# Kernel optimization log

Hardware: AMD Instinct MI355X
Metric: run time of the kernel (lower is better)

## Reference

```python
import jax, jax.numpy as jnp
import numpy as np

ALPHA = 0.2  # LeakyReLU negative slope


def setup_inputs() -> dict:
    key = jax.random.key(0)
    ks = jax.random.split(key, 7)
    N, D, O, R = 50000, 128, 128, 64
    E1, E2 = 800000, 200000
    return {
        "input": jax.random.normal(ks[0], (N, D), jnp.float32),
        "edge": jax.random.randint(ks[1], (2, E1), 0, N),
        "edge_embed": jax.random.normal(ks[2], (E1, R), jnp.float32),
        "edge_list_nhop": jax.random.randint(ks[3], (2, E2), 0, N),
        "edge_embed_nhop": jax.random.normal(ks[4], (E2, R), jnp.float32),
        "a": jax.random.normal(ks[5], (O, 2 * D + R), jnp.float32) * 0.05,
        "a_2": jax.random.normal(ks[6], (1, O), jnp.float32) * 0.05,
    }


def _gat_forward(x, edge, e_embed, a, a_2):
    N, D = x.shape
    src, dst = edge[0], edge[1]
    # a @ [x_src; x_dst; e_embed]^T computed blockwise (avoids [E, 2D+R] concat)
    a_src, a_dst, a_rel = a[:, :D], a[:, D:2 * D], a[:, 2 * D:]
    edge_m = x[src] @ a_src.T + x[dst] @ a_dst.T + e_embed @ a_rel.T  # [E, O] == edge_m^T
    score = edge_m @ a_2[0]                                            # [E]
    powers = -jnp.where(score > 0, score, ALPHA * score)               # -LeakyReLU
    edge_e = jnp.exp(powers)                                           # [E]
    e_rowsum = jax.ops.segment_sum(edge_e, src, num_segments=N)[:, None]  # [N, 1]
    e_rowsum = jnp.where(e_rowsum == 0.0, 1e-12, e_rowsum)
    edge_w = edge_e[:, None] * edge_m                                  # [E, O]
    h_prime = jax.ops.segment_sum(edge_w, src, num_segments=N)         # [N, O]
    h_prime = h_prime / e_rowsum
    return jax.nn.elu(h_prime)  # concat=True path


def reference(input, edge, edge_embed, edge_list_nhop, edge_embed_nhop, a, a_2):
    edge_all = jnp.concatenate([edge, edge_list_nhop], axis=1)        # [2, E1+E2]
    embed_all = jnp.concatenate([edge_embed, edge_embed_nhop], axis=0)  # [E1+E2, R]
    return _gat_forward(input, edge_all, embed_all, a, a_2)
```

## Files before the change

kernel.cpp:

```cpp
#include <hip/hip_runtime.h>
#include <hip/hip_bf16.h>

#define LRELU_ALPHA 0.2f

typedef __bf16 bf16x8 __attribute__((ext_vector_type(8)));
typedef float f32x4 __attribute__((ext_vector_type(4)));

__device__ __forceinline__ float waveReduceSum(float v) {
#pragma unroll
    for (int off = 32; off > 0; off >>= 1)
        v += __shfl_xor(v, off, 64);
    return v;
}

__global__ void k_prep(const float* __restrict__ a, const float* __restrict__ a2,
                       float* __restrict__ vall, __hip_bfloat16* __restrict__ ABf) {
    int idx = blockIdx.x * 256 + threadIdx.x;
    if (idx < 128 * 320) ABf[idx] = __float2bfloat16(a[idx]);
    if (idx < 320) {
        float s = 0.f;
#pragma unroll 8
        for (int o = 0; o < 128; ++o) s += a[o * 320 + idx] * a2[o];
        vall[idx] = s;
    }
}

__global__ void k_node_scores(const float* __restrict__ x, const float* __restrict__ vall,
                              float* __restrict__ s_src, float* __restrict__ s_dst,
                              __hip_bfloat16* __restrict__ XBf, int N) {
    int wid = (int)((blockIdx.x * (size_t)blockDim.x + threadIdx.x) >> 6);
    int lane = threadIdx.x & 63;
    if (wid >= N) return;
    const float* xp = x + (size_t)wid * 128;
    float x0 = xp[lane], x1 = xp[lane + 64];
    XBf[(size_t)wid * 128 + lane]      = __float2bfloat16(x0);
    XBf[(size_t)wid * 128 + 64 + lane] = __float2bfloat16(x1);
    float ps = x0 * vall[lane] + x1 * vall[lane + 64];
    float pd = x0 * vall[128 + lane] + x1 * vall[192 + lane];
    ps = waveReduceSum(ps);
    pd = waveReduceSum(pd);
    if (lane == 0) { s_src[wid] = ps; s_dst[wid] = pd; }
}

__global__ void k_count(const int* __restrict__ e1, int E1, const int* __restrict__ e2, int E2,
                        int* __restrict__ cnt) {
    int e = blockIdx.x * blockDim.x + threadIdx.x;
    if (e >= E1 + E2) return;
    int src = (e < E1) ? e1[e] : e2[e - E1];
    atomicAdd(&cnt[src], 1);
}

__global__ void k_scan1(const int* __restrict__ cnt, int* __restrict__ bsum, int N) {
    __shared__ int red[256];
    int t = threadIdx.x;
    int idx = blockIdx.x * 256 + t;
    red[t] = (idx < N) ? cnt[idx] : 0;
    __syncthreads();
    for (int off = 128; off > 0; off >>= 1) {
        if (t < off) red[t] += red[t + off];
        __syncthreads();
    }
    if (t == 0) bsum[blockIdx.x] = red[0];
}

__global__ void k_scan2(int* __restrict__ bsum, int nb) {
    __shared__ int tmp[256];
    int t = threadIdx.x;
    int v = (t < nb) ? bsum[t] : 0;
    tmp[t] = v;
    __syncthreads();
    for (int off = 1; off < 256; off <<= 1) {
        int add = (t >= off) ? tmp[t - off] : 0;
        __syncthreads();
        tmp[t] += add;
        __syncthreads();
    }
    if (t < nb) bsum[t] = tmp[t] - v;
}

__global__ void k_scan3(const int* __restrict__ cnt, const int* __restrict__ bsum,
                        int* __restrict__ start, int* __restrict__ cursor, int N, int E) {
    __shared__ int tmp[256];
    int t = threadIdx.x;
    int idx = blockIdx.x * 256 + t;
    int v = (idx < N) ? cnt[idx] : 0;
    tmp[t] = v;
    __syncthreads();
    for (int off = 1; off < 256; off <<= 1) {
        int add = (t >= off) ? tmp[t - off] : 0;
        __syncthreads();
        tmp[t] += add;
        __syncthreads();
    }
    if (idx < N) {
        int excl = tmp[t] - v + bsum[blockIdx.x];
        start[idx] = excl;
        cursor[idx] = excl;
    }
    if (blockIdx.x == 0 && t == 0) start[N] = E;
}

__global__ void k_scatter(const int* __restrict__ e1, int E1, const int* __restrict__ e2, int E2,
                          int* __restrict__ cursor, int2* __restrict__ se) {
    int e = blockIdx.x * blockDim.x + threadIdx.x;
    if (e >= E1 + E2) return;
    int src, dst;
    if (e < E1) { src = e1[e]; dst = e1[E1 + e]; }
    else { int t = e - E1; src = e2[t]; dst = e2[E2 + t]; }
    int p = atomicAdd(&cursor[src], 1);
    se[p] = make_int2(dst, e);
}

__global__ void k_gather(const __hip_bfloat16* __restrict__ XBf,
                         const float* __restrict__ emb1, const float* __restrict__ emb2, int E1,
                         const int* __restrict__ start, const int2* __restrict__ se,
                         const float* __restrict__ vall,
                         const float* __restrict__ s_src, const float* __restrict__ s_dst,
                         __hip_bfloat16* __restrict__ G, float* __restrict__ sxf, int N) {
    int n = (int)((blockIdx.x * (size_t)blockDim.x + threadIdx.x) >> 6);
    int lane = threadIdx.x & 63;
    if (n >= N) return;
    n = __builtin_amdgcn_readfirstlane(n);
    int b = start[n], en = start[n + 1];
    float r2l = vall[256 + lane];
    float ssrc = s_src[n];
    float ux = 0.f, uy = 0.f, w0 = 0.f, rs = 0.f;
    int p = b;
    for (; p + 1 < en; p += 2) {
        int2 d0 = se[p], d1 = se[p + 1];
        const float* ep0 = (d0.y < E1) ? emb1 + (size_t)d0.y * 64 : emb2 + (size_t)(d0.y - E1) * 64;
        const float* ep1 = (d1.y < E1) ? emb1 + (size_t)d1.y * 64 : emb2 + (size_t)(d1.y - E1) * 64;
        float em0 = ep0[lane], em1 = ep1[lane];
        __hip_bfloat162 xv0 = *reinterpret_cast<const __hip_bfloat162*>(XBf + (size_t)d0.x * 128 + 2 * lane);
        __hip_bfloat162 xv1 = *reinterpret_cast<const __hip_bfloat162*>(XBf + (size_t)d1.x * 128 + 2 * lane);
        float sd0 = s_dst[d0.x], sd1 = s_dst[d1.x];
        float t0 = em0 * r2l, t1 = em1 * r2l;
#pragma unroll
        for (int off = 32; off > 0; off >>= 1) {
            t0 += __shfl_xor(t0, off, 64);
            t1 += __shfl_xor(t1, off, 64);
        }
        float sc0 = ssrc + sd0 + t0;
        float sc1 = ssrc + sd1 + t1;
        float pz0 = sc0 > 0.f ? sc0 : LRELU_ALPHA * sc0;
        float pz1 = sc1 > 0.f ? sc1 : LRELU_ALPHA * sc1;
        float e0 = __expf(-pz0), e1v = __expf(-pz1);
        ux += e0 * __bfloat162float(xv0.x); uy += e0 * __bfloat162float(xv0.y);
        w0 += e0 * em0; rs += e0;
        ux += e1v * __bfloat162float(xv1.x); uy += e1v * __bfloat162float(xv1.y);
        w0 += e1v * em1; rs += e1v;
    }
    if (p < en) {
        int2 d0 = se[p];
        const float* ep0 = (d0.y < E1) ? emb1 + (size_t)d0.y * 64 : emb2 + (size_t)(d0.y - E1) * 64;
        float em0 = ep0[lane];
        __hip_bfloat162 xv0 = *reinterpret_cast<const __hip_bfloat162*>(XBf + (size_t)d0.x * 128 + 2 * lane);
        float sd0 = s_dst[d0.x];
        float t0 = waveReduceSum(em0 * r2l);
        float sc0 = ssrc + sd0 + t0;
        float pz0 = sc0 > 0.f ? sc0 : LRELU_ALPHA * sc0;
        float e0 = __expf(-pz0);
        ux += e0 * __bfloat162float(xv0.x); uy += e0 * __bfloat162float(xv0.y);
        w0 += e0 * em0; rs += e0;
    }
    float inv = (rs == 0.f) ? 0.f : 1.f / rs;
    __hip_bfloat16* gp = G + (size_t)n * 192;
    __hip_bfloat162 uv;
    uv.x = __float2bfloat16(ux * inv);
    uv.y = __float2bfloat16(uy * inv);
    *reinterpret_cast<__hip_bfloat162*>(gp + 2 * lane) = uv;
    gp[128 + lane] = __float2bfloat16(w0 * inv);
    if (lane == 0) sxf[n] = (rs == 0.f) ? 0.f : 1.f;
}

__global__ __launch_bounds__(256) void k_mfma(
    const __hip_bfloat16* __restrict__ XBf, const __hip_bfloat16* __restrict__ G,
    const __hip_bfloat16* __restrict__ ABf, const float* __restrict__ sxf,
    float* __restrict__ out, int N) {
    int lane = threadIdx.x & 63;
    int wave = threadIdx.x >> 6;
    int m0 = blockIdx.x * 64 + wave * 16;
    int q = lane >> 4, m = lane & 15;
    int rowm = m0 + m; if (rowm >= N) rowm = N - 1;
    const __hip_bfloat16* xr = XBf + (size_t)rowm * 128 + q * 8;
    const __hip_bfloat16* gr = G + (size_t)rowm * 192 + q * 8;
    const __hip_bfloat16* br = ABf + (size_t)m * 320 + q * 8;
    f32x4 acc[8];
#pragma unroll
    for (int c = 0; c < 8; ++c) acc[c] = f32x4{0.f, 0.f, 0.f, 0.f};

#pragma unroll
    for (int s = 0; s < 4; ++s) {
        bf16x8 af = *reinterpret_cast<const bf16x8*>(xr + s * 32);
#pragma unroll
        for (int c = 0; c < 8; ++c) {
            bf16x8 bf = *reinterpret_cast<const bf16x8*>(br + (size_t)c * 16 * 320 + s * 32);
            acc[c] = __builtin_amdgcn_mfma_f32_16x16x32_bf16(af, bf, acc[c], 0, 0, 0);
        }
    }
#pragma unroll
    for (int s = 0; s < 6; ++s) {
        bf16x8 af = *reinterpret_cast<const bf16x8*>(gr + s * 32);
#pragma unroll
        for (int c = 0; c < 8; ++c) {
            bf16x8 bf = *reinterpret_cast<const bf16x8*>(br + (size_t)c * 16 * 320 + 128 + s * 32);
            acc[c] = __builtin_amdgcn_mfma_f32_16x16x32_bf16(af, bf, acc[c], 0, 0, 0);
        }
    }

    float sxr[4];
#pragma unroll
    for (int r = 0; r < 4; ++r) {
        int n = m0 + q * 4 + r;
        sxr[r] = (n < N) ? sxf[n] : 0.f;
    }
#pragma unroll
    for (int c = 0; c < 8; ++c) {
#pragma unroll
        for (int r = 0; r < 4; ++r) {
            int n = m0 + q * 4 + r;
            if (n < N) {
                float h = acc[c][r] * sxr[r];
                out[(size_t)n * 128 + c * 16 + m] = h > 0.f ? h : __expf(h) - 1.f;
            }
        }
    }
}

extern "C" void kernel_launch(void* const* d_in, const int* in_sizes, int n_in,
                              void* d_out, int out_size, void* d_ws, size_t ws_size,
                              hipStream_t stream) {
    const float* x    = (const float*)d_in[0];
    const int*   e1   = (const int*)d_in[1];
    const float* emb1 = (const float*)d_in[2];
    const int*   e2   = (const int*)d_in[3];
    const float* emb2 = (const float*)d_in[4];
    const float* a    = (const float*)d_in[5];
    const float* a2   = (const float*)d_in[6];
    float* out = (float*)d_out;

    const int N  = in_sizes[0] / 128;
    const int E1 = in_sizes[1] / 2;
    const int E2 = in_sizes[3] / 2;
    const int E  = E1 + E2;
    const int NB = (N + 255) / 256;

    float* ws    = (float*)d_ws;
    float* vall  = ws;
    __hip_bfloat16* ABf = (__hip_bfloat16*)(ws + 512);
    float* s_src = ws + 512 + 20480;
    float* s_dst = s_src + N;
    float* sxf   = s_dst + N;
    int*   cnt    = (int*)(sxf + N);
    int*   bsum   = cnt + N;
    int*   start  = bsum + 256;
    int*   cursor = start + N + 1;
    size_t so = (size_t)((char*)(cursor + N + 1) - (char*)d_ws);
    so = (so + 15) & ~(size_t)15;
    int2*  se = (int2*)((char*)d_ws + so);
    size_t xo = so + (size_t)E * sizeof(int2);
    xo = (xo + 15) & ~(size_t)15;
    __hip_bfloat16* XBf = (__hip_bfloat16*)((char*)d_ws + xo);
    size_t go = xo + (size_t)N * 128 * sizeof(__hip_bfloat16);
    go = (go + 15) & ~(size_t)15;
    __hip_bfloat16* G = (__hip_bfloat16*)((char*)d_ws + go);

    size_t needed = go + (size_t)N * 192 * sizeof(__hip_bfloat16);
    if (ws_size < needed) return;

    hipMemsetAsync(cnt, 0, (size_t)N * sizeof(int), stream);

    k_prep<<<(128 * 320 + 255) / 256, 256, 0, stream>>>(a, a2, vall, ABf);
    k_node_scores<<<(N * 64 + 255) / 256, 256, 0, stream>>>(x, vall, s_src, s_dst, XBf, N);
    k_count<<<(E + 255) / 256, 256, 0, stream>>>(e1, E1, e2, E2, cnt);
    k_scan1<<<NB, 256, 0, stream>>>(cnt, bsum, N);
    k_scan2<<<1, 256, 0, stream>>>(bsum, NB);
    k_scan3<<<NB, 256, 0, stream>>>(cnt, bsum, start, cursor, N, E);
    k_scatter<<<(E + 255) / 256, 256, 0, stream>>>(e1, E1, e2, E2, cursor, se);
    k_gather<<<(N * 64 + 255) / 256, 256, 0, stream>>>(
        XBf, emb1, emb2, E1, start, se, vall, s_src, s_dst, G, sxf, N);
    k_mfma<<<(N + 63) / 64, 256, 0, stream>>>(XBf, G, ABf, sxf, out, N);
}
```

Measured before the change: 566.3 us.

## Split gather wave into four 16-lane groups processing edges in parallel

The per-node gather kernel now assigns each 16-lane quarter of the wave to a different edge. Each lane loads vectorized chunks (8 bf16 of x, 4 floats of the embedding), so one wave handles 8 edges per iteration instead of 2. The score reduction becomes a 4-step shuffle within the 16-lane group, and a cross-group shuffle reduction runs at the end. This targets memory-level parallelism and shuffle cost, in exchange for more registers, padded edge slots masked to zero on low-degree nodes, and stores made only by 16 lanes.

```diff
diff --git a/kernel.cpp b/kernel.cpp
--- a/kernel.cpp
+++ b/kernel.cpp
@@ -4,6 +4,7 @@
 #define LRELU_ALPHA 0.2f
 
 typedef __bf16 bf16x8 __attribute__((ext_vector_type(8)));
+typedef __bf16 bf16x4 __attribute__((ext_vector_type(4)));
 typedef float f32x4 __attribute__((ext_vector_type(4)));
 
 __device__ __forceinline__ float waveReduceSum(float v) {
@@ -121,22 +122,33 @@
     int lane = threadIdx.x & 63;
     if (n >= N) return;
     n = __builtin_amdgcn_readfirstlane(n);
+    int g = lane >> 4;
+    int t = lane & 15;
     int b = start[n], en = start[n + 1];
-    float r2l = vall[256 + lane];
     float ssrc = s_src[n];
-    float ux = 0.f, uy = 0.f, w0 = 0.f, rs = 0.f;
-    int p = b;
-    for (; p + 1 < en; p += 2) {
-        int2 d0 = se[p], d1 = se[p + 1];
+    f32x4 r4 = *reinterpret_cast<const f32x4*>(vall + 256 + 4 * t);
+    f32x4 w4 = {0.f, 0.f, 0.f, 0.f};
+    float u8[8] = {0.f, 0.f, 0.f, 0.f, 0.f, 0.f, 0.f, 0.f};
+    float rs = 0.f;
+
+    for (int p = b; p < en; p += 8) {
+        int q0 = p + g;
+        int q1 = p + 4 + g;
+        int c0 = (q0 < en) ? q0 : en - 1;
+        int c1 = (q1 < en) ? q1 : en - 1;
+        int2 d0 = se[c0];
+        int2 d1 = se[c1];
         const float* ep0 = (d0.y < E1) ? emb1 + (size_t)d0.y * 64 : emb2 + (size_t)(d0.y - E1) * 64;
         const float* ep1 = (d1.y < E1) ? emb1 + (size_t)d1.y * 64 : emb2 + (size_t)(d1.y - E1) * 64;
-        float em0 = ep0[lane], em1 = ep1[lane];
-        __hip_bfloat162 xv0 = *reinterpret_cast<const __hip_bfloat162*>(XBf + (size_t)d0.x * 128 + 2 * lane);
-        __hip_bfloat162 xv1 = *reinterpret_cast<const __hip_bfloat162*>(XBf + (size_t)d1.x * 128 + 2 * lane);
+        f32x4 em0 = *reinterpret_cast<const f32x4*>(ep0 + 4 * t);
+        f32x4 em1 = *reinterpret_cast<const f32x4*>(ep1 + 4 * t);
+        bf16x8 xv0 = *reinterpret_cast<const bf16x8*>(XBf + (size_t)d0.x * 128 + 8 * t);
+        bf16x8 xv1 = *reinterpret_cast<const bf16x8*>(XBf + (size_t)d1.x * 128 + 8 * t);
         float sd0 = s_dst[d0.x], sd1 = s_dst[d1.x];
-        float t0 = em0 * r2l, t1 = em1 * r2l;
-#pragma unroll
-        for (int off = 32; off > 0; off >>= 1) {
+        float t0 = em0.x * r4.x + em0.y * r4.y + em0.z * r4.z + em0.w * r4.w;
+        float t1 = em1.x * r4.x + em1.y * r4.y + em1.z * r4.z + em1.w * r4.w;
+#pragma unroll
+        for (int off = 1; off <= 8; off <<= 1) {
             t0 += __shfl_xor(t0, off, 64);
             t1 += __shfl_xor(t1, off, 64);
         }
@@ -144,33 +156,43 @@
         float sc1 = ssrc + sd1 + t1;
         float pz0 = sc0 > 0.f ? sc0 : LRELU_ALPHA * sc0;
         float pz1 = sc1 > 0.f ? sc1 : LRELU_ALPHA * sc1;
-        float e0 = __expf(-pz0), e1v = __expf(-pz1);
-        ux += e0 * __bfloat162float(xv0.x); uy += e0 * __bfloat162float(xv0.y);
-        w0 += e0 * em0; rs += e0;
-        ux += e1v * __bfloat162float(xv1.x); uy += e1v * __bfloat162float(xv1.y);
-        w0 += e1v * em1; rs += e1v;
-    }
-    if (p < en) {
-        int2 d0 = se[p];
-        const float* ep0 = (d0.y < E1) ? emb1 + (size_t)d0.y * 64 : emb2 + (size_t)(d0.y - E1) * 64;
-        float em0 = ep0[lane];
-        __hip_bfloat162 xv0 = *reinterpret_cast<const __hip_bfloat162*>(XBf + (size_t)d0.x * 128 + 2 * lane);
-        float sd0 = s_dst[d0.x];
-        float t0 = waveReduceSum(em0 * r2l);
-        float sc0 = ssrc + sd0 + t0;
-        float pz0 = sc0 > 0.f ? sc0 : LRELU_ALPHA * sc0;
         float e0 = __expf(-pz0);
-        ux += e0 * __bfloat162float(xv0.x); uy += e0 * __bfloat162float(xv0.y);
-        w0 += e0 * em0; rs += e0;
-    }
+        float e1v = __expf(-pz1);
+        if (q0 >= en) e0 = 0.f;
+        if (q1 >= en) e1v = 0.f;
+        rs += e0 + e1v;
+        w4 += e0 * em0 + e1v * em1;
+#pragma unroll
+        for (int j = 0; j < 8; ++j)
+            u8[j] += e0 * (float)xv0[j] + e1v * (float)xv1[j];
+    }
+
+#pragma unroll
+    for (int j = 0; j < 8; ++j) {
+        u8[j] += __shfl_xor(u8[j], 16, 64);
+        u8[j] += __shfl_xor(u8[j], 32, 64);
+    }
+#pragma unroll
+    for (int j = 0; j < 4; ++j) {
+        w4[j] += __shfl_xor(w4[j], 16, 64);
+        w4[j] += __shfl_xor(w4[j], 32, 64);
+    }
+    rs += __shfl_xor(rs, 16, 64);
+    rs += __shfl_xor(rs, 32, 64);
+
     float inv = (rs == 0.f) ? 0.f : 1.f / rs;
-    __hip_bfloat16* gp = G + (size_t)n * 192;
-    __hip_bfloat162 uv;
-    uv.x = __float2bfloat16(ux * inv);
-    uv.y = __float2bfloat16(uy * inv);
-    *reinterpret_cast<__hip_bfloat162*>(gp + 2 * lane) = uv;
-    gp[128 + lane] = __float2bfloat16(w0 * inv);
-    if (lane == 0) sxf[n] = (rs == 0.f) ? 0.f : 1.f;
+    if (lane < 16) {
+        __hip_bfloat16* gp = G + (size_t)n * 192;
+        bf16x8 uu;
+#pragma unroll
+        for (int j = 0; j < 8; ++j) uu[j] = (__bf16)(u8[j] * inv);
+        *reinterpret_cast<bf16x8*>(gp + 8 * lane) = uu;
+        bf16x4 ww;
+#pragma unroll
+        for (int j = 0; j < 4; ++j) ww[j] = (__bf16)(w4[j] * inv);
+        *reinterpret_cast<bf16x4*>(gp + 128 + 4 * lane) = ww;
+        if (lane == 0) sxf[n] = (rs == 0.f) ? 0.f : 1.f;
+    }
 }
 
 __global__ __launch_bounds__(256) void k_mfma(
```

Result: no change. 557.1 us (-1.6%).
